# Optimization experiments

Hardware: AMD Instinct MI355X
Metric: run time of the kernel (lower is better)

The kernel has to match this reference:

```python
import jax, jax.numpy as jnp
import numpy as np

D_MODEL = 1024
NUM_HEAD = 16
D_HEAD = D_MODEL // NUM_HEAD
NEG_INF = -1e9


def setup_inputs() -> dict:
    key = jax.random.key(0)
    ks = jax.random.split(key, 10)
    B, S = 16, 512
    v = jax.random.normal(ks[0], (B, S, D_MODEL), dtype=jnp.float32)
    lengths = jax.random.randint(ks[1], (B,), 1, S + 1, dtype=jnp.int32)
    scale = 0.02
    Wq = jax.random.normal(ks[2], (D_MODEL, D_MODEL), dtype=jnp.float32) * scale
    bq = jnp.zeros((D_MODEL,), dtype=jnp.float32)
    Wk = jax.random.normal(ks[3], (D_MODEL, D_MODEL), dtype=jnp.float32) * scale
    bk = jnp.zeros((D_MODEL,), dtype=jnp.float32)
    Wv = jax.random.normal(ks[4], (D_MODEL, D_MODEL), dtype=jnp.float32) * scale
    bv = jnp.zeros((D_MODEL,), dtype=jnp.float32)
    Wo = jax.random.normal(ks[5], (D_MODEL, D_MODEL), dtype=jnp.float32) * scale
    bo = jnp.zeros((D_MODEL,), dtype=jnp.float32)
    return {"v": v, "lengths": lengths, "Wq": Wq, "bq": bq, "Wk": Wk,
            "bk": bk, "Wv": Wv, "bv": bv, "Wo": Wo, "bo": bo}


def reference(v, lengths, Wq, bq, Wk, bk, Wv, bv, Wo, bo):
    B, S, D = v.shape
    H, Dh = NUM_HEAD, D_HEAD
    # key-padding mask: True where key position j is valid (j < lengths[b])
    valid = jnp.arange(S)[None, :] < lengths[:, None]          # [B, S]
    # project q, k, v and split heads -> [B, H, S, Dh]
    def split_heads(x):
        return x.reshape(B, S, H, Dh).transpose(0, 2, 1, 3)
    q = split_heads(v @ Wq + bq)
    k = split_heads(v @ Wk + bk)
    val = split_heads(v @ Wv + bv)
    scores = jnp.einsum('bhqd,bhkd->bhqk', q, k) / jnp.sqrt(jnp.float32(Dh))
    scores = jnp.where(valid[:, None, None, :], scores, NEG_INF)  # mask padded keys
    attn = jax.nn.softmax(scores, axis=-1)
    out = jnp.einsum('bhqk,bhkd->bhqd', attn, val)              # [B, H, S, Dh]
    out = out.transpose(0, 2, 1, 3).reshape(B, S, D)
    return out @ Wo + bo
```

## Files before the change

### kernel.cpp

```cpp
#include <hip/hip_runtime.h>
#include <hip/hip_bf16.h>

typedef unsigned short u16;
typedef unsigned int u32;
typedef __attribute__((ext_vector_type(8))) short short8;
typedef __attribute__((ext_vector_type(4))) float f32x4;
typedef __attribute__((ext_vector_type(4))) unsigned int u32x4;

#define B_SZ 16
#define S_SZ 512
#define D_SZ 1024
#define H_SZ 16
#define DH_SZ 64
#define M_SZ (B_SZ * S_SZ)
#define EXPSCALE 0.18033688f

__device__ __forceinline__ void gload_lds16(const void* g, void* l) {
  __builtin_amdgcn_global_load_lds(
      (const __attribute__((address_space(1))) unsigned int*)g,
      (__attribute__((address_space(3))) unsigned int*)l,
      16, 0, 0);
}

__device__ __forceinline__ u16 bf16b(float x) {
  __hip_bfloat16 h = __float2bfloat16(x);
  return *(u16*)&h;
}

__global__ __launch_bounds__(256) void prep(
    const float* __restrict__ v, u16* __restrict__ vB,
    const float* __restrict__ W0, const float* __restrict__ W1,
    const float* __restrict__ W2, const float* __restrict__ W3,
    u16* __restrict__ T0, u16* __restrict__ T1,
    u16* __restrict__ T2, u16* __restrict__ T3) {
  __shared__ float tile[32][33];
  const int bid = blockIdx.x;
  if (bid < 8192) {
    int i = bid * 256 + threadIdx.x;
    const float4 f = *(const float4*)&v[(size_t)i * 4];
    ushort4 o;
    o.x = bf16b(f.x); o.y = bf16b(f.y); o.z = bf16b(f.z); o.w = bf16b(f.w);
    *(ushort4*)&vB[(size_t)i * 4] = o;
    return;
  }
  const int tb = bid - 8192;
  const int z = tb >> 10, rem = tb & 1023;
  const int by = rem >> 5, bx = rem & 31;
  const float* W; u16* T;
  switch (z) {
    case 0: W = W0; T = T0; break;
    case 1: W = W1; T = T1; break;
    case 2: W = W2; T = T2; break;
    default: W = W3; T = T3; break;
  }
  int tx = threadIdx.x & 31, ty = threadIdx.x >> 5;
  int x = bx * 32 + tx;
#pragma unroll
  for (int i = 0; i < 32; i += 8)
    tile[ty + i][tx] = W[(size_t)(by * 32 + ty + i) * 1024 + x];
  __syncthreads();
  int x2 = by * 32 + tx;
#pragma unroll
  for (int i = 0; i < 32; i += 8)
    T[(size_t)(bx * 32 + ty + i) * 1024 + x2] = bf16b(tile[tx][ty + i]);
}

struct G8 {
  const u16* A; const u16* Bt;
  u16* As; u16* Bs;
  int m0, n0;
  int wave, c, quad, r7, wm, wn;
  int srow, slc8;
};

#define AS_T (128 * 64)
#define BS_T (256 * 64)

__device__ __forceinline__ void stage_a(const G8& g, int buf, int kt, int i) {
  const int grp = g.wave * 2 + i;
  gload_lds16(&g.A[(size_t)(g.m0 + grp * 8 + g.srow) * 1024 + kt * 64 + g.slc8],
              g.As + buf * AS_T + grp * 512);
}
__device__ __forceinline__ void stage_b(const G8& g, int buf, int kt, int i) {
  const int grp = g.wave * 4 + i;
  gload_lds16(&g.Bt[(size_t)(g.n0 + grp * 8 + g.srow) * 1024 + kt * 64 + g.slc8],
              g.Bs + buf * BS_T + grp * 512);
}

template<bool ST, int VM>
__device__ __forceinline__ void tile_step(const G8& g, int cur, int stg, int kt2,
                                          f32x4 acc[4][4]) {
  const u16* ab = g.As + cur * AS_T;
  const u16* bb = g.Bs + cur * BS_T;
  short8 af0[4], bf0[4], af1[4], bf1[4];

  const int pc0 = (g.quad ^ g.r7) * 8;
  const int pc1 = ((4 + g.quad) ^ g.r7) * 8;
#pragma unroll
  for (int i = 0; i < 4; ++i) {
    af0[i] = *(const short8*)&ab[(g.wm + i * 16 + g.c) * 64 + pc0];
    bf0[i] = *(const short8*)&bb[(g.wn + i * 16 + g.c) * 64 + pc0];
    af1[i] = *(const short8*)&ab[(g.wm + i * 16 + g.c) * 64 + pc1];
    bf1[i] = *(const short8*)&bb[(g.wn + i * 16 + g.c) * 64 + pc1];
  }
  if constexpr (ST) {
    stage_a(g, stg, kt2, 0);
    stage_a(g, stg, kt2, 1);
    stage_b(g, stg, kt2, 0);
    stage_b(g, stg, kt2, 1);
    stage_b(g, stg, kt2, 2);
    stage_b(g, stg, kt2, 3);
  }
  __builtin_amdgcn_s_setprio(1);
#pragma unroll
  for (int mi = 0; mi < 4; ++mi)
#pragma unroll
    for (int ni = 0; ni < 4; ++ni)
      acc[mi][ni] = __builtin_amdgcn_mfma_f32_16x16x32_bf16(
          af0[mi], bf0[ni], acc[mi][ni], 0, 0, 0);
#pragma unroll
  for (int mi = 0; mi < 4; ++mi)
#pragma unroll
    for (int ni = 0; ni < 4; ++ni)
      acc[mi][ni] = __builtin_amdgcn_mfma_f32_16x16x32_bf16(
          af1[mi], bf1[ni], acc[mi][ni], 0, 0, 0);
  __builtin_amdgcn_s_setprio(0);
  if constexpr (VM == 6) {
    asm volatile("s_waitcnt vmcnt(6)" ::: "memory");
    __builtin_amdgcn_s_barrier();
  } else if constexpr (VM == 0) {
    asm volatile("s_waitcnt vmcnt(0)" ::: "memory");
    __builtin_amdgcn_s_barrier();
  }
}

__device__ __forceinline__ void gemm_core8(
    const u16* __restrict__ A, const u16* __restrict__ Bt,
    u16* AsB, u16* BsB, int m0, int n0, f32x4 acc[4][4]) {
  const int tid = threadIdx.x;
  const int lane = tid & 63;
  G8 g;
  g.A = A; g.Bt = Bt; g.As = AsB; g.Bs = BsB;
  g.m0 = m0; g.n0 = n0;
  g.wave = tid >> 6;
  g.c = lane & 15; g.quad = lane >> 4; g.r7 = g.c & 7;
  g.wm = (g.wave >> 2) * 64;
  g.wn = (g.wave & 3) * 64;
  g.srow = lane >> 3;
  g.slc8 = ((lane & 7) ^ g.srow) * 8;

  stage_a(g, 0, 0, 0); stage_a(g, 0, 0, 1);
  stage_b(g, 0, 0, 0); stage_b(g, 0, 0, 1); stage_b(g, 0, 0, 2); stage_b(g, 0, 0, 3);
  stage_a(g, 1, 1, 0); stage_a(g, 1, 1, 1);
  stage_b(g, 1, 1, 0); stage_b(g, 1, 1, 1); stage_b(g, 1, 1, 2); stage_b(g, 1, 1, 3);
  asm volatile("s_waitcnt vmcnt(6)" ::: "memory");
  __builtin_amdgcn_s_barrier();

  int cur = 0, stg = 2;
#pragma unroll 1
  for (int t = 0; t < 14; ++t) {
    tile_step<true, 6>(g, cur, stg, t + 2, acc);
    cur = (cur == 2) ? 0 : cur + 1;
    stg = (stg == 2) ? 0 : stg + 1;
  }
  tile_step<false, 0>(g, cur, 0, 0, acc);
  tile_step<false, -1>(g, 0, 0, 0, acc);
}

__global__ __launch_bounds__(512, 2) void gemm_qkv(
    const u16* __restrict__ A,
    const u16* __restrict__ BtQ, const u16* __restrict__ BtK, const u16* __restrict__ BtV,
    const float* __restrict__ bq, const float* __restrict__ bk, const float* __restrict__ bv,
    const int* __restrict__ lengths,
    u16* __restrict__ Qo, u16* __restrict__ Kt, u16* __restrict__ Vt) {
  __shared__ u16 As[3][AS_T];
  __shared__ u16 Bs[3][BS_T];
  const int z = blockIdx.z;
  const int m0 = blockIdx.x * 128, n0 = blockIdx.y * 256;

  if (z != 0) {
    const int bb = m0 >> 9, s0 = m0 & 511;
    const int kmaxb = (lengths[bb] + 63) & ~63;
    if (s0 >= kmaxb) return;
  }

  const u16* Bt = (z == 0) ? BtQ : (z == 1) ? BtK : BtV;
  const float* bias = (z == 0) ? bq : (z == 1) ? bk : bv;

  f32x4 acc[4][4];
#pragma unroll
  for (int i = 0; i < 4; ++i)
#pragma unroll
    for (int j = 0; j < 4; ++j) acc[i][j] = f32x4{0.f, 0.f, 0.f, 0.f};

  gemm_core8(A, Bt, &As[0][0], &Bs[0][0], m0, n0, acc);

  const int lane = threadIdx.x & 63, wave = threadIdx.x >> 6;
  const int wm = (wave >> 2) * 64, wn = (wave & 3) * 64;
  const int c = lane & 15, quad = lane >> 4;
#pragma unroll
  for (int ni = 0; ni < 4; ++ni) {
    int n = n0 + wn + ni * 16 + c;
    float bval = bias[n];
#pragma unroll
    for (int mi = 0; mi < 4; ++mi) {
      int mb = m0 + wm + mi * 16 + quad * 4;
      if (z == 2) {
        int bb = mb >> 9, s = mb & 511, hh = n >> 6, d = n & 63;
        ushort4 st;
        st.x = bf16b(acc[mi][ni][0] + bval);
        st.y = bf16b(acc[mi][ni][1] + bval);
        st.z = bf16b(acc[mi][ni][2] + bval);
        st.w = bf16b(acc[mi][ni][3] + bval);
        *(ushort4*)&Vt[(((size_t)(bb * 16 + hh) * 64 + d) << 9) + s] = st;
      } else if (z == 0) {
#pragma unroll
        for (int r = 0; r < 4; ++r) {
          int m = mb + r;
          Qo[(size_t)m * 1024 + n] = bf16b((acc[mi][ni][r] + bval) * EXPSCALE);
        }
      } else {
#pragma unroll
        for (int r = 0; r < 4; ++r) {
          int m = mb + r;
          int bb = m >> 9, s = m & 511, hh = n >> 6, d = n & 63;
          Kt[(((size_t)(bb * 16 + hh) * 512 + s) << 6) + d] = bf16b(acc[mi][ni][r] + bval);
        }
      }
    }
  }
}

__global__ __launch_bounds__(512, 2) void gemm_out(
    const u16* __restrict__ A, const u16* __restrict__ Bt,
    const float* __restrict__ bias, float* __restrict__ Cf) {
  __shared__ u16 As[3][AS_T];
  __shared__ u16 Bs[3][BS_T];
  const int m0 = blockIdx.x * 128, n0 = blockIdx.y * 256;

  f32x4 acc[4][4];
#pragma unroll
  for (int i = 0; i < 4; ++i)
#pragma unroll
    for (int j = 0; j < 4; ++j) acc[i][j] = f32x4{0.f, 0.f, 0.f, 0.f};

  gemm_core8(A, Bt, &As[0][0], &Bs[0][0], m0, n0, acc);

  const int lane = threadIdx.x & 63, wave = threadIdx.x >> 6;
  const int wm = (wave >> 2) * 64, wn = (wave & 3) * 64;
  const int c = lane & 15, quad = lane >> 4;
#pragma unroll
  for (int ni = 0; ni < 4; ++ni) {
    int n = n0 + wn + ni * 16 + c;
    float bval = bias[n];
#pragma unroll
    for (int mi = 0; mi < 4; ++mi) {
#pragma unroll
      for (int r = 0; r < 4; ++r) {
        int m = m0 + wm + mi * 16 + quad * 4 + r;
        Cf[(size_t)m * 1024 + n] = acc[mi][ni][r] + bval;
      }
    }
  }
}

__global__ __launch_bounds__(256) void attn_v10(
    const u16* __restrict__ Q, const u16* __restrict__ Kt,
    const u16* __restrict__ Vt, const int* __restrict__ lengths,
    u16* __restrict__ O) {
  const int qc = blockIdx.x, h = blockIdx.y, b = blockIdx.z;
  const int t = threadIdx.x;
  const int lane = t & 63, wave = t >> 6;
  const int c = lane & 15, quad = lane >> 4;
  const int len = lengths[b];
  const int q0 = qc * 64 + wave * 16;

  __shared__ __align__(16) u16 Ks[64 * 64];
  __shared__ __align__(16) u16 Vs[64 * 64];

  const size_t bBase = (size_t)b * (S_SZ * D_SZ);
  const size_t hBase = ((size_t)(b * H_SZ + h)) * (S_SZ * DH_SZ);

  short8 aq0 = *(const short8*)&Q[bBase + (size_t)(q0 + c) * 1024 + h * 64 + quad * 8];
  short8 aq1 = *(const short8*)&Q[bBase + (size_t)(q0 + c) * 1024 + h * 64 + 32 + quad * 8];

  const short ONE = (short)0x3F80;
  const short8 ones = {ONE, ONE, ONE, ONE, ONE, ONE, ONE, ONE};

  const int srow = lane >> 3;
  const int slc = (lane & 7) ^ srow;

  f32x4 o[4];
  f32x4 osum = {0.f, 0.f, 0.f, 0.f};
#pragma unroll
  for (int i = 0; i < 4; ++i) o[i] = f32x4{0.f, 0.f, 0.f, 0.f};

  const int kmax = (len + 63) & ~63;
  for (int k0 = 0; k0 < kmax; k0 += 64) {
    __syncthreads();
#pragma unroll
    for (int g = 0; g < 2; ++g) {
      const int grp = wave * 2 + g;
      const int rho = grp * 8 + srow;
      const int grow = ((rho >> 4) & 1) * 32 + ((rho >> 2) & 3) * 8 +
                       ((rho >> 5) & 1) * 4 + (rho & 3);
      gload_lds16(&Kt[hBase + (size_t)(k0 + grow) * 64 + slc * 8],
                  &Ks[grp * 512]);
      gload_lds16(&Vt[hBase + (size_t)(grp * 8 + srow) * 512 + k0 + slc * 8],
                  &Vs[grp * 512]);
    }
    __syncthreads();

    const bool full = (k0 + 64 <= len);

#pragma unroll
    for (int half = 0; half < 2; ++half) {
      u32 pk[4];
#pragma unroll
      for (int ss = 0; ss < 2; ++ss) {
        const int sub = half + ss * 2;
        const int row = sub * 16 + c;
        short8 bk0 = *(const short8*)&Ks[row * 64 + ((quad ^ (c & 7))) * 8];
        short8 bk1 = *(const short8*)&Ks[row * 64 + (((4 + quad) ^ (c & 7))) * 8];
        const int keyb = k0 + (sub & 1) * 32 + quad * 8 + (sub >> 1) * 4;
        f32x4 s = {0.f, 0.f, 0.f, 0.f};
        s = __builtin_amdgcn_mfma_f32_16x16x32_bf16(bk0, aq0, s, 0, 0, 0);
        s = __builtin_amdgcn_mfma_f32_16x16x32_bf16(bk1, aq1, s, 0, 0, 0);
        float p0, p1, p2, p3;
        if (full) {
          p0 = exp2f(s[0]); p1 = exp2f(s[1]);
          p2 = exp2f(s[2]); p3 = exp2f(s[3]);
        } else {
          p0 = (keyb + 0) < len ? exp2f(s[0]) : 0.f;
          p1 = (keyb + 1) < len ? exp2f(s[1]) : 0.f;
          p2 = (keyb + 2) < len ? exp2f(s[2]) : 0.f;
          p3 = (keyb + 3) < len ? exp2f(s[3]) : 0.f;
        }
        pk[ss * 2 + 0] = (u32)bf16b(p0) | ((u32)bf16b(p1) << 16);
        pk[ss * 2 + 1] = (u32)bf16b(p2) | ((u32)bf16b(p3) << 16);
      }
      u32x4 w0 = {pk[0], pk[1], pk[2], pk[3]};
      short8 pa;
      __builtin_memcpy(&pa, &w0, 16);
      osum = __builtin_amdgcn_mfma_f32_16x16x32_bf16(pa, ones, osum, 0, 0, 0);
#pragma unroll
      for (int dt = 0; dt < 4; ++dt) {
        const int vrow = dt * 16 + c;
        short8 vb = *(const short8*)&Vs[vrow * 64 + (((half * 4 + quad) ^ (c & 7))) * 8];
        o[dt] = __builtin_amdgcn_mfma_f32_16x16x32_bf16(pa, vb, o[dt], 0, 0, 0);
      }
    }
  }

  float inv[4];
#pragma unroll
  for (int r = 0; r < 4; ++r) inv[r] = 1.0f / osum[r];
#pragma unroll
  for (int dt = 0; dt < 4; ++dt) {
#pragma unroll
    for (int r = 0; r < 4; ++r) {
      int s = q0 + quad * 4 + r;
      float val = o[dt][r] * inv[r];
      O[bBase + (size_t)s * 1024 + h * 64 + dt * 16 + c] = bf16b(val);
    }
  }
}

extern "C" void kernel_launch(void* const* d_in, const int* in_sizes, int n_in,
                              void* d_out, int out_size, void* d_ws, size_t ws_size,
                              hipStream_t stream) {
  const float* v  = (const float*)d_in[0];
  const int* lengths = (const int*)d_in[1];
  const float* Wq = (const float*)d_in[2];
  const float* bq = (const float*)d_in[3];
  const float* Wk = (const float*)d_in[4];
  const float* bk = (const float*)d_in[5];
  const float* Wv = (const float*)d_in[6];
  const float* bv = (const float*)d_in[7];
  const float* Wo = (const float*)d_in[8];
  const float* bo = (const float*)d_in[9];

  char* ws = (char*)d_ws;
  const size_t TSZ = (size_t)M_SZ * D_SZ * 2;
  const size_t WSZ = (size_t)1 << 21;
  u16* vB  = (u16*)(ws);
  u16* AO  = vB;
  u16* WqT = (u16*)(ws + TSZ + 0 * WSZ);
  u16* WkT = (u16*)(ws + TSZ + 1 * WSZ);
  u16* WvT = (u16*)(ws + TSZ + 2 * WSZ);
  u16* WoT = (u16*)(ws + TSZ + 3 * WSZ);
  u16* Qb  = (u16*)(ws + TSZ + 4 * WSZ + 0 * TSZ);
  u16* Kt  = (u16*)(ws + TSZ + 4 * WSZ + 1 * TSZ);
  u16* Vt  = (u16*)(ws + TSZ + 4 * WSZ + 2 * TSZ);

  prep<<<dim3(8192 + 4096), 256, 0, stream>>>(v, vB, Wq, Wk, Wv, Wo, WqT, WkT, WvT, WoT);

  gemm_qkv<<<dim3(64, 4, 3), 512, 0, stream>>>(vB, WqT, WkT, WvT, bq, bk, bv, lengths, Qb, Kt, Vt);

  attn_v10<<<dim3(8, 16, 16), 256, 0, stream>>>(Qb, Kt, Vt, lengths, AO);

  gemm_out<<<dim3(64, 4), 512, 0, stream>>>(AO, WoT, bo, (float*)d_out);
}
```

Baseline: 217.2 us.

## Enlarge GEMM tiles to 256x256 with double-buffered LDS pipeline

The QKV and output projection GEMMs move from 128x256 block tiles with a 3-stage LDS ring to 256x256 tiles with a 2-stage double buffer. Each wave now computes a 128x64 sub-tile with 32 accumulators, and fragment loads are split into two k-halves to limit register pressure. The aim is higher arithmetic intensity and fewer global loads per FLOP. The costs are half as many blocks (less parallelism and coarser length-based skipping in the K/V projection), a shallower prefetch pipeline with a full vmcnt(0) wait every step, and higher register use.

```diff
diff --git a/kernel.cpp b/kernel.cpp
--- a/kernel.cpp
+++ b/kernel.cpp
@@ -65,7 +65,7 @@
     T[(size_t)(bx * 32 + ty + i) * 1024 + x2] = bf16b(tile[tx][ty + i]);
 }
 
-struct G8 {
+struct G256 {
   const u16* A; const u16* Bt;
   u16* As; u16* Bs;
   int m0, n0;
@@ -73,98 +73,93 @@
   int srow, slc8;
 };
 
-#define AS_T (128 * 64)
-#define BS_T (256 * 64)
-
-__device__ __forceinline__ void stage_a(const G8& g, int buf, int kt, int i) {
-  const int grp = g.wave * 2 + i;
-  gload_lds16(&g.A[(size_t)(g.m0 + grp * 8 + g.srow) * 1024 + kt * 64 + g.slc8],
-              g.As + buf * AS_T + grp * 512);
-}
-__device__ __forceinline__ void stage_b(const G8& g, int buf, int kt, int i) {
-  const int grp = g.wave * 4 + i;
-  gload_lds16(&g.Bt[(size_t)(g.n0 + grp * 8 + g.srow) * 1024 + kt * 64 + g.slc8],
-              g.Bs + buf * BS_T + grp * 512);
-}
-
-template<bool ST, int VM>
-__device__ __forceinline__ void tile_step(const G8& g, int cur, int stg, int kt2,
-                                          f32x4 acc[4][4]) {
-  const u16* ab = g.As + cur * AS_T;
-  const u16* bb = g.Bs + cur * BS_T;
-  short8 af0[4], bf0[4], af1[4], bf1[4];
-
+#define AS4_T (256 * 64)
+#define BS4_T (256 * 64)
+
+__device__ __forceinline__ void stage256(const G256& g, int buf, int kt) {
+#pragma unroll
+  for (int i = 0; i < 4; ++i) {
+    const int grp = g.wave * 4 + i;
+    gload_lds16(&g.A[(size_t)(g.m0 + grp * 8 + g.srow) * 1024 + kt * 64 + g.slc8],
+                g.As + buf * AS4_T + grp * 512);
+  }
+#pragma unroll
+  for (int i = 0; i < 4; ++i) {
+    const int grp = g.wave * 4 + i;
+    gload_lds16(&g.Bt[(size_t)(g.n0 + grp * 8 + g.srow) * 1024 + kt * 64 + g.slc8],
+                g.Bs + buf * BS4_T + grp * 512);
+  }
+}
+
+template<bool ST>
+__device__ __forceinline__ void tile_step256(const G256& g, int cur, int kt2,
+                                             f32x4 acc[8][4]) {
+  const u16* ab = g.As + cur * AS4_T;
+  const u16* bb = g.Bs + cur * BS4_T;
   const int pc0 = (g.quad ^ g.r7) * 8;
   const int pc1 = ((4 + g.quad) ^ g.r7) * 8;
-#pragma unroll
-  for (int i = 0; i < 4; ++i) {
-    af0[i] = *(const short8*)&ab[(g.wm + i * 16 + g.c) * 64 + pc0];
-    bf0[i] = *(const short8*)&bb[(g.wn + i * 16 + g.c) * 64 + pc0];
-    af1[i] = *(const short8*)&ab[(g.wm + i * 16 + g.c) * 64 + pc1];
-    bf1[i] = *(const short8*)&bb[(g.wn + i * 16 + g.c) * 64 + pc1];
-  }
-  if constexpr (ST) {
-    stage_a(g, stg, kt2, 0);
-    stage_a(g, stg, kt2, 1);
-    stage_b(g, stg, kt2, 0);
-    stage_b(g, stg, kt2, 1);
-    stage_b(g, stg, kt2, 2);
-    stage_b(g, stg, kt2, 3);
-  }
+
+  short8 af[8], bf[4];
+#pragma unroll
+  for (int i = 0; i < 8; ++i)
+    af[i] = *(const short8*)&ab[(g.wm + i * 16 + g.c) * 64 + pc0];
+#pragma unroll
+  for (int i = 0; i < 4; ++i)
+    bf[i] = *(const short8*)&bb[(g.wn + i * 16 + g.c) * 64 + pc0];
+  if constexpr (ST) stage256(g, cur ^ 1, kt2);
   __builtin_amdgcn_s_setprio(1);
 #pragma unroll
-  for (int mi = 0; mi < 4; ++mi)
+  for (int mi = 0; mi < 8; ++mi)
 #pragma unroll
     for (int ni = 0; ni < 4; ++ni)
       acc[mi][ni] = __builtin_amdgcn_mfma_f32_16x16x32_bf16(
-          af0[mi], bf0[ni], acc[mi][ni], 0, 0, 0);
-#pragma unroll
-  for (int mi = 0; mi < 4; ++mi)
+          af[mi], bf[ni], acc[mi][ni], 0, 0, 0);
+  __builtin_amdgcn_s_setprio(0);
+
+#pragma unroll
+  for (int i = 0; i < 8; ++i)
+    af[i] = *(const short8*)&ab[(g.wm + i * 16 + g.c) * 64 + pc1];
+#pragma unroll
+  for (int i = 0; i < 4; ++i)
+    bf[i] = *(const short8*)&bb[(g.wn + i * 16 + g.c) * 64 + pc1];
+  __builtin_amdgcn_s_setprio(1);
+#pragma unroll
+  for (int mi = 0; mi < 8; ++mi)
 #pragma unroll
     for (int ni = 0; ni < 4; ++ni)
       acc[mi][ni] = __builtin_amdgcn_mfma_f32_16x16x32_bf16(
-          af1[mi], bf1[ni], acc[mi][ni], 0, 0, 0);
+          af[mi], bf[ni], acc[mi][ni], 0, 0, 0);
   __builtin_amdgcn_s_setprio(0);
-  if constexpr (VM == 6) {
-    asm volatile("s_waitcnt vmcnt(6)" ::: "memory");
-    __builtin_amdgcn_s_barrier();
-  } else if constexpr (VM == 0) {
+
+  if constexpr (ST) {
     asm volatile("s_waitcnt vmcnt(0)" ::: "memory");
     __builtin_amdgcn_s_barrier();
   }
 }
 
-__device__ __forceinline__ void gemm_core8(
+__device__ __forceinline__ void gemm_core256(
     const u16* __restrict__ A, const u16* __restrict__ Bt,
-    u16* AsB, u16* BsB, int m0, int n0, f32x4 acc[4][4]) {
+    u16* AsB, u16* BsB, int m0, int n0, f32x4 acc[8][4]) {
   const int tid = threadIdx.x;
   const int lane = tid & 63;
-  G8 g;
+  G256 g;
   g.A = A; g.Bt = Bt; g.As = AsB; g.Bs = BsB;
   g.m0 = m0; g.n0 = n0;
   g.wave = tid >> 6;
   g.c = lane & 15; g.quad = lane >> 4; g.r7 = g.c & 7;
-  g.wm = (g.wave >> 2) * 64;
+  g.wm = (g.wave >> 2) * 128;
   g.wn = (g.wave & 3) * 64;
   g.srow = lane >> 3;
   g.slc8 = ((lane & 7) ^ g.srow) * 8;
 
-  stage_a(g, 0, 0, 0); stage_a(g, 0, 0, 1);
-  stage_b(g, 0, 0, 0); stage_b(g, 0, 0, 1); stage_b(g, 0, 0, 2); stage_b(g, 0, 0, 3);
-  stage_a(g, 1, 1, 0); stage_a(g, 1, 1, 1);
-  stage_b(g, 1, 1, 0); stage_b(g, 1, 1, 1); stage_b(g, 1, 1, 2); stage_b(g, 1, 1, 3);
-  asm volatile("s_waitcnt vmcnt(6)" ::: "memory");
+  stage256(g, 0, 0);
+  asm volatile("s_waitcnt vmcnt(0)" ::: "memory");
   __builtin_amdgcn_s_barrier();
 
-  int cur = 0, stg = 2;
 #pragma unroll 1
-  for (int t = 0; t < 14; ++t) {
-    tile_step<true, 6>(g, cur, stg, t + 2, acc);
-    cur = (cur == 2) ? 0 : cur + 1;
-    stg = (stg == 2) ? 0 : stg + 1;
-  }
-  tile_step<false, 0>(g, cur, 0, 0, acc);
-  tile_step<false, -1>(g, 0, 0, 0, acc);
+  for (int t = 0; t < 15; ++t)
+    tile_step256<true>(g, t & 1, t + 1, acc);
+  tile_step256<false>(g, 15 & 1, 0, acc);
 }
 
 __global__ __launch_bounds__(512, 2) void gemm_qkv(
@@ -173,10 +168,10 @@
     const float* __restrict__ bq, const float* __restrict__ bk, const float* __restrict__ bv,
     const int* __restrict__ lengths,
     u16* __restrict__ Qo, u16* __restrict__ Kt, u16* __restrict__ Vt) {
-  __shared__ u16 As[3][AS_T];
-  __shared__ u16 Bs[3][BS_T];
+  __shared__ u16 As[2][AS4_T];
+  __shared__ u16 Bs[2][BS4_T];
   const int z = blockIdx.z;
-  const int m0 = blockIdx.x * 128, n0 = blockIdx.y * 256;
+  const int m0 = blockIdx.x * 256, n0 = blockIdx.y * 256;
 
   if (z != 0) {
     const int bb = m0 >> 9, s0 = m0 & 511;
@@ -187,23 +182,23 @@
   const u16* Bt = (z == 0) ? BtQ : (z == 1) ? BtK : BtV;
   const float* bias = (z == 0) ? bq : (z == 1) ? bk : bv;
 
-  f32x4 acc[4][4];
-#pragma unroll
-  for (int i = 0; i < 4; ++i)
+  f32x4 acc[8][4];
+#pragma unroll
+  for (int i = 0; i < 8; ++i)
 #pragma unroll
     for (int j = 0; j < 4; ++j) acc[i][j] = f32x4{0.f, 0.f, 0.f, 0.f};
 
-  gemm_core8(A, Bt, &As[0][0], &Bs[0][0], m0, n0, acc);
+  gemm_core256(A, Bt, &As[0][0], &Bs[0][0], m0, n0, acc);
 
   const int lane = threadIdx.x & 63, wave = threadIdx.x >> 6;
-  const int wm = (wave >> 2) * 64, wn = (wave & 3) * 64;
+  const int wm = (wave >> 2) * 128, wn = (wave & 3) * 64;
   const int c = lane & 15, quad = lane >> 4;
 #pragma unroll
   for (int ni = 0; ni < 4; ++ni) {
     int n = n0 + wn + ni * 16 + c;
     float bval = bias[n];
 #pragma unroll
-    for (int mi = 0; mi < 4; ++mi) {
+    for (int mi = 0; mi < 8; ++mi) {
       int mb = m0 + wm + mi * 16 + quad * 4;
       if (z == 2) {
         int bb = mb >> 9, s = mb & 511, hh = n >> 6, d = n & 63;
@@ -234,27 +229,27 @@
 __global__ __launch_bounds__(512, 2) void gemm_out(
     const u16* __restrict__ A, const u16* __restrict__ Bt,
     const float* __restrict__ bias, float* __restrict__ Cf) {
-  __shared__ u16 As[3][AS_T];
-  __shared__ u16 Bs[3][BS_T];
-  const int m0 = blockIdx.x * 128, n0 = blockIdx.y * 256;
-
-  f32x4 acc[4][4];
-#pragma unroll
-  for (int i = 0; i < 4; ++i)
+  __shared__ u16 As[2][AS4_T];
+  __shared__ u16 Bs[2][BS4_T];
+  const int m0 = blockIdx.x * 256, n0 = blockIdx.y * 256;
+
+  f32x4 acc[8][4];
+#pragma unroll
+  for (int i = 0; i < 8; ++i)
 #pragma unroll
     for (int j = 0; j < 4; ++j) acc[i][j] = f32x4{0.f, 0.f, 0.f, 0.f};
 
-  gemm_core8(A, Bt, &As[0][0], &Bs[0][0], m0, n0, acc);
+  gemm_core256(A, Bt, &As[0][0], &Bs[0][0], m0, n0, acc);
 
   const int lane = threadIdx.x & 63, wave = threadIdx.x >> 6;
-  const int wm = (wave >> 2) * 64, wn = (wave & 3) * 64;
+  const int wm = (wave >> 2) * 128, wn = (wave & 3) * 64;
   const int c = lane & 15, quad = lane >> 4;
 #pragma unroll
   for (int ni = 0; ni < 4; ++ni) {
     int n = n0 + wn + ni * 16 + c;
     float bval = bias[n];
 #pragma unroll
-    for (int mi = 0; mi < 4; ++mi) {
+    for (int mi = 0; mi < 8; ++mi) {
 #pragma unroll
       for (int r = 0; r < 4; ++r) {
         int m = m0 + wm + mi * 16 + quad * 4 + r;
@@ -395,9 +390,9 @@
 
   prep<<<dim3(8192 + 4096), 256, 0, stream>>>(v, vB, Wq, Wk, Wv, Wo, WqT, WkT, WvT, WoT);
 
-  gemm_qkv<<<dim3(64, 4, 3), 512, 0, stream>>>(vB, WqT, WkT, WvT, bq, bk, bv, lengths, Qb, Kt, Vt);
+  gemm_qkv<<<dim3(32, 4, 3), 512, 0, stream>>>(vB, WqT, WkT, WvT, bq, bk, bv, lengths, Qb, Kt, Vt);
 
   attn_v10<<<dim3(8, 16, 16), 256, 0, stream>>>(Qb, Kt, Vt, lengths, AO);
 
-  gemm_out<<<dim3(64, 4), 512, 0, stream>>>(AO, WoT, bo, (float*)d_out);
-}
+  gemm_out<<<dim3(32, 4), 512, 0, stream>>>(AO, WoT, bo, (float*)d_out);
+}
```

Result: slower. 235.9 us (+8.6%).

## Drop LDS staging in attention and process two query tiles per wave

Applied to the files above, without the earlier changes.

The attention kernel no longer stages K and V tiles through shared memory with barriers. Each wave now reads K and V fragments straight from global memory, relying on L1/L2, and computes two 16-row query tiles per wave, so each loaded K/V fragment feeds twice as many MFMAs. The grid is halved to 4 query chunks of 128 rows. This removes the syncthreads and LDS round trips but adds per-wave global loads that the four waves of a block no longer share, plus more register pressure and fewer blocks for the GPU to schedule.

```diff
diff --git a/kernel.cpp b/kernel.cpp
--- a/kernel.cpp
+++ b/kernel.cpp
@@ -264,7 +264,7 @@
   }
 }
 
-__global__ __launch_bounds__(256) void attn_v10(
+__global__ __launch_bounds__(256) void attn_v11(
     const u16* __restrict__ Q, const u16* __restrict__ Kt,
     const u16* __restrict__ Vt, const int* __restrict__ lengths,
     u16* __restrict__ O) {
@@ -273,95 +273,97 @@
   const int lane = t & 63, wave = t >> 6;
   const int c = lane & 15, quad = lane >> 4;
   const int len = lengths[b];
-  const int q0 = qc * 64 + wave * 16;
-
-  __shared__ __align__(16) u16 Ks[64 * 64];
-  __shared__ __align__(16) u16 Vs[64 * 64];
+  const int q0 = qc * 128 + wave * 32;
 
   const size_t bBase = (size_t)b * (S_SZ * D_SZ);
   const size_t hBase = ((size_t)(b * H_SZ + h)) * (S_SZ * DH_SZ);
 
-  short8 aq0 = *(const short8*)&Q[bBase + (size_t)(q0 + c) * 1024 + h * 64 + quad * 8];
-  short8 aq1 = *(const short8*)&Q[bBase + (size_t)(q0 + c) * 1024 + h * 64 + 32 + quad * 8];
+  short8 aq[2][2];
+#pragma unroll
+  for (int qt = 0; qt < 2; ++qt) {
+    aq[qt][0] = *(const short8*)&Q[bBase + (size_t)(q0 + qt * 16 + c) * 1024 + h * 64 + quad * 8];
+    aq[qt][1] = *(const short8*)&Q[bBase + (size_t)(q0 + qt * 16 + c) * 1024 + h * 64 + 32 + quad * 8];
+  }
 
   const short ONE = (short)0x3F80;
   const short8 ones = {ONE, ONE, ONE, ONE, ONE, ONE, ONE, ONE};
 
-  const int srow = lane >> 3;
-  const int slc = (lane & 7) ^ srow;
-
-  f32x4 o[4];
-  f32x4 osum = {0.f, 0.f, 0.f, 0.f};
-#pragma unroll
-  for (int i = 0; i < 4; ++i) o[i] = f32x4{0.f, 0.f, 0.f, 0.f};
+  f32x4 o[2][4];
+  f32x4 osum[2];
+#pragma unroll
+  for (int qt = 0; qt < 2; ++qt) {
+    osum[qt] = f32x4{0.f, 0.f, 0.f, 0.f};
+#pragma unroll
+    for (int i = 0; i < 4; ++i) o[qt][i] = f32x4{0.f, 0.f, 0.f, 0.f};
+  }
 
   const int kmax = (len + 63) & ~63;
+#pragma unroll 1
   for (int k0 = 0; k0 < kmax; k0 += 64) {
-    __syncthreads();
-#pragma unroll
-    for (int g = 0; g < 2; ++g) {
-      const int grp = wave * 2 + g;
-      const int rho = grp * 8 + srow;
-      const int grow = ((rho >> 4) & 1) * 32 + ((rho >> 2) & 3) * 8 +
-                       ((rho >> 5) & 1) * 4 + (rho & 3);
-      gload_lds16(&Kt[hBase + (size_t)(k0 + grow) * 64 + slc * 8],
-                  &Ks[grp * 512]);
-      gload_lds16(&Vt[hBase + (size_t)(grp * 8 + srow) * 512 + k0 + slc * 8],
-                  &Vs[grp * 512]);
-    }
-    __syncthreads();
-
     const bool full = (k0 + 64 <= len);
 
 #pragma unroll
     for (int half = 0; half < 2; ++half) {
-      u32 pk[4];
+      u32 pk[2][4];
 #pragma unroll
       for (int ss = 0; ss < 2; ++ss) {
         const int sub = half + ss * 2;
         const int row = sub * 16 + c;
-        short8 bk0 = *(const short8*)&Ks[row * 64 + ((quad ^ (c & 7))) * 8];
-        short8 bk1 = *(const short8*)&Ks[row * 64 + (((4 + quad) ^ (c & 7))) * 8];
+        const int grow = ((row >> 4) & 1) * 32 + ((row >> 2) & 3) * 8 +
+                         ((row >> 5) & 1) * 4 + (row & 3);
+        const u16* kp = &Kt[hBase + (size_t)(k0 + grow) * 64];
+        short8 bk0 = *(const short8*)&kp[quad * 8];
+        short8 bk1 = *(const short8*)&kp[32 + quad * 8];
         const int keyb = k0 + (sub & 1) * 32 + quad * 8 + (sub >> 1) * 4;
-        f32x4 s = {0.f, 0.f, 0.f, 0.f};
-        s = __builtin_amdgcn_mfma_f32_16x16x32_bf16(bk0, aq0, s, 0, 0, 0);
-        s = __builtin_amdgcn_mfma_f32_16x16x32_bf16(bk1, aq1, s, 0, 0, 0);
-        float p0, p1, p2, p3;
-        if (full) {
-          p0 = exp2f(s[0]); p1 = exp2f(s[1]);
-          p2 = exp2f(s[2]); p3 = exp2f(s[3]);
-        } else {
-          p0 = (keyb + 0) < len ? exp2f(s[0]) : 0.f;
-          p1 = (keyb + 1) < len ? exp2f(s[1]) : 0.f;
-          p2 = (keyb + 2) < len ? exp2f(s[2]) : 0.f;
-          p3 = (keyb + 3) < len ? exp2f(s[3]) : 0.f;
+#pragma unroll
+        for (int qt = 0; qt < 2; ++qt) {
+          f32x4 s = {0.f, 0.f, 0.f, 0.f};
+          s = __builtin_amdgcn_mfma_f32_16x16x32_bf16(bk0, aq[qt][0], s, 0, 0, 0);
+          s = __builtin_amdgcn_mfma_f32_16x16x32_bf16(bk1, aq[qt][1], s, 0, 0, 0);
+          float p0, p1, p2, p3;
+          if (full) {
+            p0 = exp2f(s[0]); p1 = exp2f(s[1]);
+            p2 = exp2f(s[2]); p3 = exp2f(s[3]);
+          } else {
+            p0 = (keyb + 0) < len ? exp2f(s[0]) : 0.f;
+            p1 = (keyb + 1) < len ? exp2f(s[1]) : 0.f;
+            p2 = (keyb + 2) < len ? exp2f(s[2]) : 0.f;
+            p3 = (keyb + 3) < len ? exp2f(s[3]) : 0.f;
+          }
+          pk[qt][ss * 2 + 0] = (u32)bf16b(p0) | ((u32)bf16b(p1) << 16);
+          pk[qt][ss * 2 + 1] = (u32)bf16b(p2) | ((u32)bf16b(p3) << 16);
         }
-        pk[ss * 2 + 0] = (u32)bf16b(p0) | ((u32)bf16b(p1) << 16);
-        pk[ss * 2 + 1] = (u32)bf16b(p2) | ((u32)bf16b(p3) << 16);
       }
-      u32x4 w0 = {pk[0], pk[1], pk[2], pk[3]};
-      short8 pa;
-      __builtin_memcpy(&pa, &w0, 16);
-      osum = __builtin_amdgcn_mfma_f32_16x16x32_bf16(pa, ones, osum, 0, 0, 0);
+      u32x4 w0 = {pk[0][0], pk[0][1], pk[0][2], pk[0][3]};
+      u32x4 w1 = {pk[1][0], pk[1][1], pk[1][2], pk[1][3]};
+      short8 pa0, pa1;
+      __builtin_memcpy(&pa0, &w0, 16);
+      __builtin_memcpy(&pa1, &w1, 16);
+      osum[0] = __builtin_amdgcn_mfma_f32_16x16x32_bf16(pa0, ones, osum[0], 0, 0, 0);
+      osum[1] = __builtin_amdgcn_mfma_f32_16x16x32_bf16(pa1, ones, osum[1], 0, 0, 0);
 #pragma unroll
       for (int dt = 0; dt < 4; ++dt) {
-        const int vrow = dt * 16 + c;
-        short8 vb = *(const short8*)&Vs[vrow * 64 + (((half * 4 + quad) ^ (c & 7))) * 8];
-        o[dt] = __builtin_amdgcn_mfma_f32_16x16x32_bf16(pa, vb, o[dt], 0, 0, 0);
+        short8 vb = *(const short8*)&Vt[hBase + (size_t)(dt * 16 + c) * 512 +
+                                        k0 + (half * 4 + quad) * 8];
+        o[0][dt] = __builtin_amdgcn_mfma_f32_16x16x32_bf16(pa0, vb, o[0][dt], 0, 0, 0);
+        o[1][dt] = __builtin_amdgcn_mfma_f32_16x16x32_bf16(pa1, vb, o[1][dt], 0, 0, 0);
       }
     }
   }
 
-  float inv[4];
-#pragma unroll
-  for (int r = 0; r < 4; ++r) inv[r] = 1.0f / osum[r];
-#pragma unroll
-  for (int dt = 0; dt < 4; ++dt) {
-#pragma unroll
-    for (int r = 0; r < 4; ++r) {
-      int s = q0 + quad * 4 + r;
-      float val = o[dt][r] * inv[r];
-      O[bBase + (size_t)s * 1024 + h * 64 + dt * 16 + c] = bf16b(val);
+#pragma unroll
+  for (int qt = 0; qt < 2; ++qt) {
+    float inv[4];
+#pragma unroll
+    for (int r = 0; r < 4; ++r) inv[r] = 1.0f / osum[qt][r];
+#pragma unroll
+    for (int dt = 0; dt < 4; ++dt) {
+#pragma unroll
+      for (int r = 0; r < 4; ++r) {
+        int s = q0 + qt * 16 + quad * 4 + r;
+        float val = o[qt][dt][r] * inv[r];
+        O[bBase + (size_t)s * 1024 + h * 64 + dt * 16 + c] = bf16b(val);
+      }
     }
   }
 }
@@ -397,7 +399,7 @@
 
   gemm_qkv<<<dim3(64, 4, 3), 512, 0, stream>>>(vB, WqT, WkT, WvT, bq, bk, bv, lengths, Qb, Kt, Vt);
 
-  attn_v10<<<dim3(8, 16, 16), 256, 0, stream>>>(Qb, Kt, Vt, lengths, AO);
+  attn_v11<<<dim3(4, 16, 16), 256, 0, stream>>>(Qb, Kt, Vt, lengths, AO);
 
   gemm_out<<<dim3(64, 4), 512, 0, stream>>>(AO, WoT, bo, (float*)d_out);
 }
```

Measured after the change: 233.3 us. 1.07x slower.
